# Kernel optimization log

Hardware: AMD Instinct MI355X
Metric: run time of the kernel (lower is better)

The kernel has to match this reference:

```python
import jax, jax.numpy as jnp
import numpy as np

D_HEAD = 128
H_Q = 16
H_K = 4
D_MODEL = 2048
B = 2
T = 2048


def setup_inputs() -> dict:
    key = jax.random.key(0)
    k1, k2, k3, k4, k5 = jax.random.split(key, 5)
    s = 0.02
    return {
        "x": jax.random.normal(k1, (B, T, D_MODEL), dtype=jnp.float32),
        "wq": jax.random.normal(k2, (D_HEAD * H_Q, D_MODEL), dtype=jnp.float32) * s,
        "wk": jax.random.normal(k3, (D_HEAD * H_K, D_MODEL), dtype=jnp.float32) * s,
        "wv": jax.random.normal(k4, (D_HEAD * H_K, D_MODEL), dtype=jnp.float32) * s,
        "wo": jax.random.normal(k5, (D_MODEL, D_HEAD * H_Q), dtype=jnp.float32) * s,
    }


def reference(x, wq, wk, wv, wo):
    Bs, Ts, _ = x.shape
    g = H_Q // H_K  # query groups per kv head
    # projections (torch Linear: y = x @ W^T)
    Q = (x @ wq.T).reshape(Bs, Ts, H_Q, D_HEAD).transpose(0, 2, 1, 3)  # [B,hq,T,d]
    K = (x @ wk.T).reshape(Bs, Ts, H_K, D_HEAD).transpose(0, 2, 1, 3)  # [B,hk,T,d]
    V = (x @ wv.T).reshape(Bs, Ts, H_K, D_HEAD).transpose(0, 2, 1, 3)  # [B,hk,T,d]
    Qg = Q.reshape(Bs, g, H_K, Ts, D_HEAD)  # [B,g,hk,T,d]
    scale = D_HEAD ** -0.5
    attn = jnp.einsum("bghtd,bhsd->bghts", Qg, K) * scale  # [B,g,hk,T,T]
    causal = jnp.tril(jnp.ones((Ts, Ts), dtype=bool))
    attn = jnp.where(causal, attn, -jnp.inf)
    attn = jax.nn.softmax(attn, axis=-1)
    out = jnp.einsum("bghts,bhsd->bghtd", attn, V)  # [B,g,hk,T,d]
    out = out.reshape(Bs, H_Q, Ts, D_HEAD).transpose(0, 2, 1, 3).reshape(Bs, Ts, H_Q * D_HEAD)
    return out @ wo.T
```

## Files before the change

kernel.cpp:

```cpp
#include <hip/hip_runtime.h>
#include <hip/hip_bf16.h>
#include <stdint.h>

#define DMODEL 2048
#define HQ 16
#define HKV 4
#define DH 128
#define SEQT 2048
#define BATCH 2

typedef __bf16 bf16x8 __attribute__((ext_vector_type(8)));
typedef float f32x4 __attribute__((ext_vector_type(4)));
typedef float f32x16 __attribute__((ext_vector_type(16)));
typedef unsigned short u16x4 __attribute__((ext_vector_type(4)));
typedef unsigned short u16x8 __attribute__((ext_vector_type(8)));

__device__ __forceinline__ unsigned short f2bf(float x) {
  __hip_bfloat16 h = __float2bfloat16(x);
  return __builtin_bit_cast(unsigned short, h);
}
__device__ __forceinline__ unsigned int pack2(float a, float b) {
  return (unsigned int)f2bf(a) | ((unsigned int)f2bf(b) << 16);
}

__device__ __forceinline__ void gload_lds16(const void* g, void* lds) {
  __builtin_amdgcn_global_load_lds(
      (const __attribute__((address_space(1))) void*)(uintptr_t)g,
      (__attribute__((address_space(3))) void*)(uint32_t)(uintptr_t)lds,
      16, 0, 0);
}

__global__ __launch_bounds__(256) void cast_all_kernel(
    const float* __restrict__ x, const float* __restrict__ wq,
    const float* __restrict__ wk, const float* __restrict__ wv,
    const float* __restrict__ wo,
    unsigned short* __restrict__ xb, unsigned short* __restrict__ wqb,
    unsigned short* __restrict__ wkb, unsigned short* __restrict__ wvb,
    unsigned short* __restrict__ wob) {
  int i = blockIdx.x * 256 + threadIdx.x;
  const float* in; unsigned short* out; int off; float s = 1.0f;
  if (i < 1048576)      { in = x;  out = xb;  off = i; }
  else if (i < 1572864) { in = wq; out = wqb; off = i - 1048576; s = 0.1275174473f; }
  else if (i < 1703936) { in = wk; out = wkb; off = i - 1572864; }
  else if (i < 1835008) { in = wv; out = wvb; off = i - 1703936; }
  else                  { in = wo; out = wob; off = i - 1835008; }
  const float4* p = reinterpret_cast<const float4*>(in) + (size_t)off * 2;
  float4 a = p[0], b = p[1];
  u16x8 o;
  o[0] = f2bf(a.x * s); o[1] = f2bf(a.y * s); o[2] = f2bf(a.z * s); o[3] = f2bf(a.w * s);
  o[4] = f2bf(b.x * s); o[5] = f2bf(b.y * s); o[6] = f2bf(b.z * s); o[7] = f2bf(b.w * s);
  *(reinterpret_cast<u16x8*>(out) + off) = o;
}

template <bool OUT_BF16>
__device__ __forceinline__ void gemm_body(
    unsigned short* As, unsigned short* Bs,
    const unsigned short* __restrict__ A, const unsigned short* __restrict__ B,
    void* __restrict__ Cv, int N, int K, int row0, int col0) {
  const int tid = threadIdx.x;
  const int wave = tid >> 6, lane = tid & 63;
  const int wr = (wave >> 1) * 64, wc = (wave & 1) * 64;
  const int l15 = lane & 15, l4 = lane >> 4;
  const int srow = wave * 32 + (lane >> 2);
  const int scol = (lane & 3) * 8;

  f32x4 acc[4][4] = {};

  for (int k0 = 0; k0 < K; k0 += 64) {
#pragma unroll
    for (int h = 0; h < 2; ++h) {
      const unsigned short* gA = A + (size_t)(row0 + srow) * K + k0 + h * 32 + scol;
      gload_lds16(gA, (char*)As + h * 8192 + wave * 2048);
      gload_lds16(gA + (size_t)16 * K, (char*)As + h * 8192 + wave * 2048 + 1024);
      const unsigned short* gB = B + (size_t)(col0 + srow) * K + k0 + h * 32 + scol;
      gload_lds16(gB, (char*)Bs + h * 8192 + wave * 2048);
      gload_lds16(gB + (size_t)16 * K, (char*)Bs + h * 8192 + wave * 2048 + 1024);
    }
    __syncthreads();

    bf16x8 af[2][4], bfr[2][4];
#pragma unroll
    for (int h = 0; h < 2; ++h)
#pragma unroll
      for (int i = 0; i < 4; ++i) {
        af[h][i]  = *reinterpret_cast<const bf16x8*>(&As[h * 4096 + (wr + i * 16 + l15) * 32 + l4 * 8]);
        bfr[h][i] = *reinterpret_cast<const bf16x8*>(&Bs[h * 4096 + (wc + i * 16 + l15) * 32 + l4 * 8]);
      }
#pragma unroll
    for (int h = 0; h < 2; ++h)
#pragma unroll
      for (int i = 0; i < 4; ++i)
#pragma unroll
        for (int j = 0; j < 4; ++j)
          acc[i][j] = __builtin_amdgcn_mfma_f32_16x16x32_bf16(af[h][i], bfr[h][j], acc[i][j], 0, 0, 0);
    __syncthreads();
  }

#pragma unroll
  for (int i = 0; i < 4; ++i) {
    const int rrow = row0 + wr + i * 16 + l4 * 4;
#pragma unroll
    for (int j = 0; j < 4; ++j) {
      const int ccol = col0 + wc + j * 16 + l15;
#pragma unroll
      for (int r = 0; r < 4; ++r) {
        const size_t idx = (size_t)(rrow + r) * N + ccol;
        if constexpr (OUT_BF16)
          ((unsigned short*)Cv)[idx] = f2bf(acc[i][j][r]);
        else
          ((float*)Cv)[idx] = acc[i][j][r];
      }
    }
  }
}

__global__ __launch_bounds__(256) void gemm_qkv(
    const unsigned short* __restrict__ xb, const unsigned short* __restrict__ wqb,
    const unsigned short* __restrict__ wkb, const unsigned short* __restrict__ wvb,
    unsigned short* __restrict__ Qb, unsigned short* __restrict__ Kb,
    unsigned short* __restrict__ VTb) {
  __shared__ alignas(16) unsigned short As[2][128 * 32];
  __shared__ alignas(16) unsigned short Bs[2][128 * 32];
  const int bid = blockIdx.x;
  if (bid < 512) {
    gemm_body<true>(&As[0][0], &Bs[0][0], xb, wqb, Qb, 2048, DMODEL,
                    (bid >> 4) * 128, (bid & 15) * 128);
  } else if (bid < 640) {
    const int r = bid - 512;
    gemm_body<true>(&As[0][0], &Bs[0][0], xb, wkb, Kb, 512, DMODEL,
                    (r >> 2) * 128, (r & 3) * 128);
  } else {
    const int r = bid - 640;
    const int tz = r & 1, ty = (r >> 1) & 15, tx = r >> 5;
    gemm_body<true>(&As[0][0], &Bs[0][0], wvb,
                    xb + (size_t)tz * SEQT * DMODEL,
                    VTb + (size_t)tz * 512 * SEQT, SEQT, DMODEL,
                    tx * 128, ty * 128);
  }
}

template <bool OUT_BF16>
__global__ __launch_bounds__(256) void gemm_bt(
    const unsigned short* __restrict__ A, const unsigned short* __restrict__ B,
    void* __restrict__ Cv, int N, int K) {
  __shared__ alignas(16) unsigned short As[2][128 * 32];
  __shared__ alignas(16) unsigned short Bs[2][128 * 32];
  gemm_body<OUT_BF16>(&As[0][0], &Bs[0][0], A, B, Cv, N, K,
                      blockIdx.x * 128, blockIdx.y * 128);
}

__device__ __forceinline__ void tile_pass(
    const char* ksb, const char* vsb, int lane, int hi, int lq,
    int kvb, int q0, const bf16x8* qf, f32x16* acc, float& mrun, float& lrun) {
  const bool s1v = (kvb + 32 <= q0);
  const bool d0 = (kvb == q0), d1 = (kvb + 32 == q0);

  f32x16 st0 = {}, st1 = {};
  __builtin_amdgcn_s_setprio(1);
#pragma unroll
  for (int dc = 0; dc < 8; ++dc) {
    bf16x8 kf = *reinterpret_cast<const bf16x8*>(ksb + dc * 1024 + lane * 16);
    st0 = __builtin_amdgcn_mfma_f32_32x32x16_bf16(kf, qf[dc], st0, 0, 0, 0);
  }
  if (s1v) {
#pragma unroll
    for (int dc = 0; dc < 8; ++dc) {
      bf16x8 kf = *reinterpret_cast<const bf16x8*>(ksb + (8 + dc) * 1024 + lane * 16);
      st1 = __builtin_amdgcn_mfma_f32_32x32x16_bf16(kf, qf[dc], st1, 0, 0, 0);
    }
  }
  __builtin_amdgcn_s_setprio(0);

  float p0[16], p1[16];
#pragma unroll
  for (int r = 0; r < 16; ++r) p0[r] = st0[r];
  if (d0) {
#pragma unroll
    for (int r = 0; r < 16; ++r) {
      const int srw = (r & 3) + 8 * (r >> 2) + 4 * hi;
      if (srw > lq) p0[r] = -INFINITY;
    }
  }
  float tmax = -INFINITY;
#pragma unroll
  for (int r = 0; r < 16; ++r) tmax = fmaxf(tmax, p0[r]);
  if (s1v) {
#pragma unroll
    for (int r = 0; r < 16; ++r) p1[r] = st1[r];
    if (d1) {
#pragma unroll
      for (int r = 0; r < 16; ++r) {
        const int srw = (r & 3) + 8 * (r >> 2) + 4 * hi;
        if (srw > lq) p1[r] = -INFINITY;
      }
    }
#pragma unroll
    for (int r = 0; r < 16; ++r) tmax = fmaxf(tmax, p1[r]);
  }
  tmax = fmaxf(tmax, __shfl_xor(tmax, 32));
  if (!__all(tmax <= mrun)) {
    const float mnew = fmaxf(mrun, tmax);
    const float fsc = __builtin_amdgcn_exp2f(mrun - mnew);
    lrun *= fsc;
#pragma unroll
    for (int dt = 0; dt < 4; ++dt)
#pragma unroll
      for (int r = 0; r < 16; ++r) acc[dt][r] *= fsc;
    mrun = mnew;
  }
  float psum = 0.f;
#pragma unroll
  for (int r = 0; r < 16; ++r) { p0[r] = __builtin_amdgcn_exp2f(p0[r] - mrun); psum += p0[r]; }
  if (s1v) {
#pragma unroll
    for (int r = 0; r < 16; ++r) { p1[r] = __builtin_amdgcn_exp2f(p1[r] - mrun); psum += p1[r]; }
  }
  psum += __shfl_xor(psum, 32);
  lrun += psum;

  union { unsigned int u[4]; bf16x8 v; } pf0, pf1, pf2, pf3;
  {
    unsigned int x0 = pack2(p0[0], p0[1]),  x1 = pack2(p0[2], p0[3]);
    unsigned int x2 = pack2(p0[4], p0[5]),  x3 = pack2(p0[6], p0[7]);
    unsigned int x4 = pack2(p0[8], p0[9]),  x5 = pack2(p0[10], p0[11]);
    unsigned int x6 = pack2(p0[12], p0[13]), x7 = pack2(p0[14], p0[15]);
    unsigned int x0s = __shfl_xor(x0, 32), x1s = __shfl_xor(x1, 32);
    unsigned int x2s = __shfl_xor(x2, 32), x3s = __shfl_xor(x3, 32);
    unsigned int x4s = __shfl_xor(x4, 32), x5s = __shfl_xor(x5, 32);
    unsigned int x6s = __shfl_xor(x6, 32), x7s = __shfl_xor(x7, 32);
    pf0.u[0] = hi ? x2s : x0;  pf0.u[1] = hi ? x3s : x1;
    pf0.u[2] = hi ? x2  : x0s; pf0.u[3] = hi ? x3  : x1s;
    pf1.u[0] = hi ? x6s : x4;  pf1.u[1] = hi ? x7s : x5;
    pf1.u[2] = hi ? x6  : x4s; pf1.u[3] = hi ? x7  : x5s;
  }
  if (s1v) {
    unsigned int x0 = pack2(p1[0], p1[1]),  x1 = pack2(p1[2], p1[3]);
    unsigned int x2 = pack2(p1[4], p1[5]),  x3 = pack2(p1[6], p1[7]);
    unsigned int x4 = pack2(p1[8], p1[9]),  x5 = pack2(p1[10], p1[11]);
    unsigned int x6 = pack2(p1[12], p1[13]), x7 = pack2(p1[14], p1[15]);
    unsigned int x0s = __shfl_xor(x0, 32), x1s = __shfl_xor(x1, 32);
    unsigned int x2s = __shfl_xor(x2, 32), x3s = __shfl_xor(x3, 32);
    unsigned int x4s = __shfl_xor(x4, 32), x5s = __shfl_xor(x5, 32);
    unsigned int x6s = __shfl_xor(x6, 32), x7s = __shfl_xor(x7, 32);
    pf2.u[0] = hi ? x2s : x0;  pf2.u[1] = hi ? x3s : x1;
    pf2.u[2] = hi ? x2  : x0s; pf2.u[3] = hi ? x3  : x1s;
    pf3.u[0] = hi ? x6s : x4;  pf3.u[1] = hi ? x7s : x5;
    pf3.u[2] = hi ? x6  : x4s; pf3.u[3] = hi ? x7  : x5s;
  }

  __builtin_amdgcn_s_setprio(1);
#pragma unroll
  for (int dt = 0; dt < 4; ++dt) {
    bf16x8 v0 = *reinterpret_cast<const bf16x8*>(vsb + (dt * 4 + 0) * 1024 + lane * 16);
    bf16x8 v1 = *reinterpret_cast<const bf16x8*>(vsb + (dt * 4 + 1) * 1024 + lane * 16);
    acc[dt] = __builtin_amdgcn_mfma_f32_32x32x16_bf16(v0, pf0.v, acc[dt], 0, 0, 0);
    acc[dt] = __builtin_amdgcn_mfma_f32_32x32x16_bf16(v1, pf1.v, acc[dt], 0, 0, 0);
  }
  if (s1v) {
#pragma unroll
    for (int dt = 0; dt < 4; ++dt) {
      bf16x8 v2 = *reinterpret_cast<const bf16x8*>(vsb + (dt * 4 + 2) * 1024 + lane * 16);
      bf16x8 v3 = *reinterpret_cast<const bf16x8*>(vsb + (dt * 4 + 3) * 1024 + lane * 16);
      acc[dt] = __builtin_amdgcn_mfma_f32_32x32x16_bf16(v2, pf2.v, acc[dt], 0, 0, 0);
      acc[dt] = __builtin_amdgcn_mfma_f32_32x32x16_bf16(v3, pf3.v, acc[dt], 0, 0, 0);
    }
  }
  __builtin_amdgcn_s_setprio(0);
}

__global__ __launch_bounds__(256, 1) void attn_kernel(
    const unsigned short* __restrict__ Q, const unsigned short* __restrict__ Kc,
    const unsigned short* __restrict__ VT, unsigned short* __restrict__ AO) {
  __shared__ alignas(16) unsigned short Ks[2][16 * 512];
  __shared__ alignas(16) unsigned short Vs[2][16 * 512];

  const int tid = threadIdx.x;
  const int wave = tid >> 6, lane = tid & 63;
  const int bid = blockIdx.x;
  const int bhk = bid & 7;
  const int pairidx = bid >> 3;
  const int b = bhk >> 2, hk = bhk & 3;
  const int h = hk + wave * 4;
  const int jl = 63 - pairidx, js = pairidx;
  const int q0l = jl * 32, q0s = js * 32;
  const int jtl = jl >> 1, jts = js >> 1;
  const int lq = lane & 31, hi = lane >> 5;

  const size_t qrowL = (size_t)(b * SEQT + q0l + lq);
  const size_t qrowS = (size_t)(b * SEQT + q0s + lq);
  bf16x8 qfL[8], qfS[8];
  {
    const unsigned short* qpL = Q + qrowL * (HQ * DH) + h * DH + hi * 8;
    const unsigned short* qpS = Q + qrowS * (HQ * DH) + h * DH + hi * 8;
#pragma unroll
    for (int dc = 0; dc < 8; ++dc) {
      qfL[dc] = *reinterpret_cast<const bf16x8*>(qpL + dc * 16);
      qfS[dc] = *reinterpret_cast<const bf16x8*>(qpS + dc * 16);
    }
  }

  f32x16 accL[4] = {}, accS[4] = {};
  float mL = -INFINITY, lL = 0.f, mS = -INFINITY, lS = 0.f;

  const unsigned short* kbase = Kc + (size_t)b * SEQT * (HKV * DH) + hk * DH;
  const unsigned short* vtb = VT + ((size_t)b * (HKV * DH) + hk * DH) * SEQT;

  auto STAGE = [&](int buf, int kvb2) {
#pragma unroll
    for (int i = 0; i < 4; ++i) {
      const int f = i * 4 + wave;
      const int sub = f >> 3, dc = f & 7;
      const unsigned short* g = kbase + (size_t)(kvb2 + sub * 32 + lq) * (HKV * DH) + dc * 16 + hi * 8;
      gload_lds16(g, (char*)Ks[buf] + f * 1024);
    }
#pragma unroll
    for (int i = 0; i < 4; ++i) {
      const int f = i * 4 + wave;
      const int dt = f >> 2, ks = f & 3;
      const unsigned short* g = vtb + (size_t)(dt * 32 + lq) * SEQT + kvb2 + ks * 16 + hi * 8;
      gload_lds16(g, (char*)Vs[buf] + f * 1024);
    }
  };

  STAGE(0, 0);
  __syncthreads();
  int cur = 0;

  for (int t = 0; t <= jtl; ++t) {
    if (t < jtl) STAGE(cur ^ 1, (t + 1) * 64);
    const char* ksb = (const char*)Ks[cur];
    const char* vsb = (const char*)Vs[cur];
    tile_pass(ksb, vsb, lane, hi, lq, t * 64, q0l, qfL, accL, mL, lL);
    if (t <= jts)
      tile_pass(ksb, vsb, lane, hi, lq, t * 64, q0s, qfS, accS, mS, lS);
    __syncthreads();
    cur ^= 1;
  }

  auto writeO = [&](const f32x16* acc, float lrun, size_t qrow) {
    const float inv = 1.f / lrun;
    unsigned short* op = AO + qrow * (HQ * DH) + h * DH;
#pragma unroll
    for (int dt = 0; dt < 4; ++dt) {
#pragma unroll
      for (int g2 = 0; g2 < 4; ++g2) {
        u16x4 w;
#pragma unroll
        for (int jj = 0; jj < 4; ++jj) w[jj] = f2bf(acc[dt][g2 * 4 + jj] * inv);
        *reinterpret_cast<u16x4*>(op + dt * 32 + g2 * 8 + 4 * hi) = w;
      }
    }
  };
  writeO(accL, lL, qrowL);
  writeO(accS, lS, qrowS);
}

extern "C" void kernel_launch(void* const* d_in, const int* in_sizes, int n_in,
                              void* d_out, int out_size, void* d_ws, size_t ws_size,
                              hipStream_t stream) {
  const float* x  = (const float*)d_in[0];
  const float* wq = (const float*)d_in[1];
  const float* wk = (const float*)d_in[2];
  const float* wv = (const float*)d_in[3];
  const float* wo = (const float*)d_in[4];
  float* out = (float*)d_out;

  const size_t N_X  = (size_t)BATCH * SEQT * DMODEL;
  const size_t N_WQ = (size_t)HQ * DH * DMODEL;
  const size_t N_WK = (size_t)HKV * DH * DMODEL;
  const size_t N_Q  = (size_t)BATCH * SEQT * HQ * DH;
  const size_t N_K  = (size_t)BATCH * SEQT * HKV * DH;

  unsigned short* xb  = (unsigned short*)d_ws;
  unsigned short* wqb = xb  + N_X;
  unsigned short* wkb = wqb + N_WQ;
  unsigned short* wvb = wkb + N_WK;
  unsigned short* wob = wvb + N_WK;
  unsigned short* Qb  = wob + N_WQ;
  unsigned short* Kb  = Qb  + N_Q;
  unsigned short* VTb = Kb  + N_K;
  unsigned short* AOb = VTb + N_K;

  cast_all_kernel<<<dim3(9216), dim3(256), 0, stream>>>(
      x, wq, wk, wv, wo, xb, wqb, wkb, wvb, wob);

  gemm_qkv<<<dim3(768), 256, 0, stream>>>(xb, wqb, wkb, wvb, Qb, Kb, VTb);
  attn_kernel<<<dim3(256, 1, 1), 256, 0, stream>>>(Qb, Kb, VTb, AOb);
  gemm_bt<false><<<dim3(32, 16, 1), 256, 0, stream>>>(AOb, wob, out, 2048, DMODEL);
}
```

Before: 211.1 us.

## Split paired-query attention blocks into single-tile blocks and load V from global

The attention kernel no longer has each block process a long and a short query tile together. It launches 512 blocks, each handling one 32-row query tile: long tiles are scheduled first and short tiles in a second round, with launch bounds raised to allow two blocks per CU. V fragments are now read directly from global memory into registers instead of being staged in LDS. The QK^T dot product is also split into two independent accumulator chains to expose more MFMA ILP. This trades the shared K/V reuse between paired tiles, plus some register headroom, for more occupancy and less LDS traffic.

New measurement: 269.6 us. 27.7% more time.

```diff
diff --git a/kernel.cpp b/kernel.cpp
--- a/kernel.cpp
+++ b/kernel.cpp
@@ -149,163 +149,38 @@
                       blockIdx.x * 128, blockIdx.y * 128);
 }
 
-__device__ __forceinline__ void tile_pass(
-    const char* ksb, const char* vsb, int lane, int hi, int lq,
-    int kvb, int q0, const bf16x8* qf, f32x16* acc, float& mrun, float& lrun) {
-  const bool s1v = (kvb + 32 <= q0);
-  const bool d0 = (kvb == q0), d1 = (kvb + 32 == q0);
-
-  f32x16 st0 = {}, st1 = {};
-  __builtin_amdgcn_s_setprio(1);
-#pragma unroll
-  for (int dc = 0; dc < 8; ++dc) {
-    bf16x8 kf = *reinterpret_cast<const bf16x8*>(ksb + dc * 1024 + lane * 16);
-    st0 = __builtin_amdgcn_mfma_f32_32x32x16_bf16(kf, qf[dc], st0, 0, 0, 0);
-  }
-  if (s1v) {
-#pragma unroll
-    for (int dc = 0; dc < 8; ++dc) {
-      bf16x8 kf = *reinterpret_cast<const bf16x8*>(ksb + (8 + dc) * 1024 + lane * 16);
-      st1 = __builtin_amdgcn_mfma_f32_32x32x16_bf16(kf, qf[dc], st1, 0, 0, 0);
-    }
-  }
-  __builtin_amdgcn_s_setprio(0);
-
-  float p0[16], p1[16];
-#pragma unroll
-  for (int r = 0; r < 16; ++r) p0[r] = st0[r];
-  if (d0) {
-#pragma unroll
-    for (int r = 0; r < 16; ++r) {
-      const int srw = (r & 3) + 8 * (r >> 2) + 4 * hi;
-      if (srw > lq) p0[r] = -INFINITY;
-    }
-  }
-  float tmax = -INFINITY;
-#pragma unroll
-  for (int r = 0; r < 16; ++r) tmax = fmaxf(tmax, p0[r]);
-  if (s1v) {
-#pragma unroll
-    for (int r = 0; r < 16; ++r) p1[r] = st1[r];
-    if (d1) {
-#pragma unroll
-      for (int r = 0; r < 16; ++r) {
-        const int srw = (r & 3) + 8 * (r >> 2) + 4 * hi;
-        if (srw > lq) p1[r] = -INFINITY;
-      }
-    }
-#pragma unroll
-    for (int r = 0; r < 16; ++r) tmax = fmaxf(tmax, p1[r]);
-  }
-  tmax = fmaxf(tmax, __shfl_xor(tmax, 32));
-  if (!__all(tmax <= mrun)) {
-    const float mnew = fmaxf(mrun, tmax);
-    const float fsc = __builtin_amdgcn_exp2f(mrun - mnew);
-    lrun *= fsc;
-#pragma unroll
-    for (int dt = 0; dt < 4; ++dt)
-#pragma unroll
-      for (int r = 0; r < 16; ++r) acc[dt][r] *= fsc;
-    mrun = mnew;
-  }
-  float psum = 0.f;
-#pragma unroll
-  for (int r = 0; r < 16; ++r) { p0[r] = __builtin_amdgcn_exp2f(p0[r] - mrun); psum += p0[r]; }
-  if (s1v) {
-#pragma unroll
-    for (int r = 0; r < 16; ++r) { p1[r] = __builtin_amdgcn_exp2f(p1[r] - mrun); psum += p1[r]; }
-  }
-  psum += __shfl_xor(psum, 32);
-  lrun += psum;
-
-  union { unsigned int u[4]; bf16x8 v; } pf0, pf1, pf2, pf3;
-  {
-    unsigned int x0 = pack2(p0[0], p0[1]),  x1 = pack2(p0[2], p0[3]);
-    unsigned int x2 = pack2(p0[4], p0[5]),  x3 = pack2(p0[6], p0[7]);
-    unsigned int x4 = pack2(p0[8], p0[9]),  x5 = pack2(p0[10], p0[11]);
-    unsigned int x6 = pack2(p0[12], p0[13]), x7 = pack2(p0[14], p0[15]);
-    unsigned int x0s = __shfl_xor(x0, 32), x1s = __shfl_xor(x1, 32);
-    unsigned int x2s = __shfl_xor(x2, 32), x3s = __shfl_xor(x3, 32);
-    unsigned int x4s = __shfl_xor(x4, 32), x5s = __shfl_xor(x5, 32);
-    unsigned int x6s = __shfl_xor(x6, 32), x7s = __shfl_xor(x7, 32);
-    pf0.u[0] = hi ? x2s : x0;  pf0.u[1] = hi ? x3s : x1;
-    pf0.u[2] = hi ? x2  : x0s; pf0.u[3] = hi ? x3  : x1s;
-    pf1.u[0] = hi ? x6s : x4;  pf1.u[1] = hi ? x7s : x5;
-    pf1.u[2] = hi ? x6  : x4s; pf1.u[3] = hi ? x7  : x5s;
-  }
-  if (s1v) {
-    unsigned int x0 = pack2(p1[0], p1[1]),  x1 = pack2(p1[2], p1[3]);
-    unsigned int x2 = pack2(p1[4], p1[5]),  x3 = pack2(p1[6], p1[7]);
-    unsigned int x4 = pack2(p1[8], p1[9]),  x5 = pack2(p1[10], p1[11]);
-    unsigned int x6 = pack2(p1[12], p1[13]), x7 = pack2(p1[14], p1[15]);
-    unsigned int x0s = __shfl_xor(x0, 32), x1s = __shfl_xor(x1, 32);
-    unsigned int x2s = __shfl_xor(x2, 32), x3s = __shfl_xor(x3, 32);
-    unsigned int x4s = __shfl_xor(x4, 32), x5s = __shfl_xor(x5, 32);
-    unsigned int x6s = __shfl_xor(x6, 32), x7s = __shfl_xor(x7, 32);
-    pf2.u[0] = hi ? x2s : x0;  pf2.u[1] = hi ? x3s : x1;
-    pf2.u[2] = hi ? x2  : x0s; pf2.u[3] = hi ? x3  : x1s;
-    pf3.u[0] = hi ? x6s : x4;  pf3.u[1] = hi ? x7s : x5;
-    pf3.u[2] = hi ? x6  : x4s; pf3.u[3] = hi ? x7  : x5s;
-  }
-
-  __builtin_amdgcn_s_setprio(1);
-#pragma unroll
-  for (int dt = 0; dt < 4; ++dt) {
-    bf16x8 v0 = *reinterpret_cast<const bf16x8*>(vsb + (dt * 4 + 0) * 1024 + lane * 16);
-    bf16x8 v1 = *reinterpret_cast<const bf16x8*>(vsb + (dt * 4 + 1) * 1024 + lane * 16);
-    acc[dt] = __builtin_amdgcn_mfma_f32_32x32x16_bf16(v0, pf0.v, acc[dt], 0, 0, 0);
-    acc[dt] = __builtin_amdgcn_mfma_f32_32x32x16_bf16(v1, pf1.v, acc[dt], 0, 0, 0);
-  }
-  if (s1v) {
-#pragma unroll
-    for (int dt = 0; dt < 4; ++dt) {
-      bf16x8 v2 = *reinterpret_cast<const bf16x8*>(vsb + (dt * 4 + 2) * 1024 + lane * 16);
-      bf16x8 v3 = *reinterpret_cast<const bf16x8*>(vsb + (dt * 4 + 3) * 1024 + lane * 16);
-      acc[dt] = __builtin_amdgcn_mfma_f32_32x32x16_bf16(v2, pf2.v, acc[dt], 0, 0, 0);
-      acc[dt] = __builtin_amdgcn_mfma_f32_32x32x16_bf16(v3, pf3.v, acc[dt], 0, 0, 0);
-    }
-  }
-  __builtin_amdgcn_s_setprio(0);
-}
-
-__global__ __launch_bounds__(256, 1) void attn_kernel(
+__global__ __launch_bounds__(256, 2) void attn_kernel(
     const unsigned short* __restrict__ Q, const unsigned short* __restrict__ Kc,
     const unsigned short* __restrict__ VT, unsigned short* __restrict__ AO) {
   __shared__ alignas(16) unsigned short Ks[2][16 * 512];
-  __shared__ alignas(16) unsigned short Vs[2][16 * 512];
 
   const int tid = threadIdx.x;
   const int wave = tid >> 6, lane = tid & 63;
   const int bid = blockIdx.x;
-  const int bhk = bid & 7;
-  const int pairidx = bid >> 3;
+  const int round = bid >> 8, pairslot = bid & 255;
+  const int bhk = pairslot & 7;
+  const int jp = pairslot >> 3;
+  const int j = round ? jp : 63 - jp;
   const int b = bhk >> 2, hk = bhk & 3;
   const int h = hk + wave * 4;
-  const int jl = 63 - pairidx, js = pairidx;
-  const int q0l = jl * 32, q0s = js * 32;
-  const int jtl = jl >> 1, jts = js >> 1;
+  const int q0 = j * 32;
+  const int jt = j >> 1;
   const int lq = lane & 31, hi = lane >> 5;
 
-  const size_t qrowL = (size_t)(b * SEQT + q0l + lq);
-  const size_t qrowS = (size_t)(b * SEQT + q0s + lq);
-  bf16x8 qfL[8], qfS[8];
-  {
-    const unsigned short* qpL = Q + qrowL * (HQ * DH) + h * DH + hi * 8;
-    const unsigned short* qpS = Q + qrowS * (HQ * DH) + h * DH + hi * 8;
-#pragma unroll
-    for (int dc = 0; dc < 8; ++dc) {
-      qfL[dc] = *reinterpret_cast<const bf16x8*>(qpL + dc * 16);
-      qfS[dc] = *reinterpret_cast<const bf16x8*>(qpS + dc * 16);
-    }
-  }
-
-  f32x16 accL[4] = {}, accS[4] = {};
-  float mL = -INFINITY, lL = 0.f, mS = -INFINITY, lS = 0.f;
+  const size_t qrow = (size_t)(b * SEQT + q0 + lq);
+  const unsigned short* qp = Q + qrow * (HQ * DH) + h * DH + hi * 8;
+  bf16x8 qf[8];
+#pragma unroll
+  for (int dc = 0; dc < 8; ++dc)
+    qf[dc] = *reinterpret_cast<const bf16x8*>(qp + dc * 16);
+
+  f32x16 acc[4] = {};
+  float mrun = -INFINITY, lrun = 0.f;
 
   const unsigned short* kbase = Kc + (size_t)b * SEQT * (HKV * DH) + hk * DH;
-  const unsigned short* vtb = VT + ((size_t)b * (HKV * DH) + hk * DH) * SEQT;
-
-  auto STAGE = [&](int buf, int kvb2) {
+  const unsigned short* vrow = VT + ((size_t)b * (HKV * DH) + hk * DH + lq) * SEQT + hi * 8;
+
+  auto STAGE_K = [&](int buf, int kvb2) {
 #pragma unroll
     for (int i = 0; i < 4; ++i) {
       const int f = i * 4 + wave;
@@ -313,46 +188,191 @@
       const unsigned short* g = kbase + (size_t)(kvb2 + sub * 32 + lq) * (HKV * DH) + dc * 16 + hi * 8;
       gload_lds16(g, (char*)Ks[buf] + f * 1024);
     }
-#pragma unroll
-    for (int i = 0; i < 4; ++i) {
-      const int f = i * 4 + wave;
-      const int dt = f >> 2, ks = f & 3;
-      const unsigned short* g = vtb + (size_t)(dt * 32 + lq) * SEQT + kvb2 + ks * 16 + hi * 8;
-      gload_lds16(g, (char*)Vs[buf] + f * 1024);
-    }
   };
 
-  STAGE(0, 0);
+  STAGE_K(0, 0);
   __syncthreads();
   int cur = 0;
 
-  for (int t = 0; t <= jtl; ++t) {
-    if (t < jtl) STAGE(cur ^ 1, (t + 1) * 64);
-    const char* ksb = (const char*)Ks[cur];
-    const char* vsb = (const char*)Vs[cur];
-    tile_pass(ksb, vsb, lane, hi, lq, t * 64, q0l, qfL, accL, mL, lL);
-    if (t <= jts)
-      tile_pass(ksb, vsb, lane, hi, lq, t * 64, q0s, qfS, accS, mS, lS);
+  for (int t = 0; t <= jt; ++t) {
+    const int kvb = t * 64;
+    const bool s1v = (kvb + 32 <= q0);
+    const bool d0 = (kvb == q0), d1 = (kvb + 32 == q0);
+
+    bf16x8 vfa[8];
+#pragma unroll
+    for (int dt = 0; dt < 4; ++dt)
+#pragma unroll
+      for (int ks = 0; ks < 2; ++ks)
+        vfa[dt * 2 + ks] = *reinterpret_cast<const bf16x8*>(
+            vrow + (size_t)dt * 32 * SEQT + kvb + ks * 16);
+
+    if (t < jt) STAGE_K(cur ^ 1, kvb + 64);
+
+    f32x16 stA = {}, stB = {}, stA1 = {}, stB1 = {};
+    __builtin_amdgcn_s_setprio(1);
+#pragma unroll
+    for (int dc = 0; dc < 4; ++dc) {
+      bf16x8 kf = *reinterpret_cast<const bf16x8*>((char*)Ks[cur] + dc * 1024 + lane * 16);
+      stA = __builtin_amdgcn_mfma_f32_32x32x16_bf16(kf, qf[dc], stA, 0, 0, 0);
+    }
+#pragma unroll
+    for (int dc = 4; dc < 8; ++dc) {
+      bf16x8 kf = *reinterpret_cast<const bf16x8*>((char*)Ks[cur] + dc * 1024 + lane * 16);
+      stB = __builtin_amdgcn_mfma_f32_32x32x16_bf16(kf, qf[dc], stB, 0, 0, 0);
+    }
+    if (s1v) {
+#pragma unroll
+      for (int dc = 0; dc < 4; ++dc) {
+        bf16x8 kf = *reinterpret_cast<const bf16x8*>((char*)Ks[cur] + (8 + dc) * 1024 + lane * 16);
+        stA1 = __builtin_amdgcn_mfma_f32_32x32x16_bf16(kf, qf[dc], stA1, 0, 0, 0);
+      }
+#pragma unroll
+      for (int dc = 4; dc < 8; ++dc) {
+        bf16x8 kf = *reinterpret_cast<const bf16x8*>((char*)Ks[cur] + (8 + dc) * 1024 + lane * 16);
+        stB1 = __builtin_amdgcn_mfma_f32_32x32x16_bf16(kf, qf[dc], stB1, 0, 0, 0);
+      }
+    }
+    __builtin_amdgcn_s_setprio(0);
+
+    bf16x8 vfb[8];
+    if (s1v) {
+#pragma unroll
+      for (int dt = 0; dt < 4; ++dt)
+#pragma unroll
+        for (int ks = 0; ks < 2; ++ks)
+          vfb[dt * 2 + ks] = *reinterpret_cast<const bf16x8*>(
+              vrow + (size_t)dt * 32 * SEQT + kvb + 32 + ks * 16);
+    }
+
+    float p0[16], p1[16];
+#pragma unroll
+    for (int r = 0; r < 16; ++r) p0[r] = stA[r] + stB[r];
+    if (d0) {
+#pragma unroll
+      for (int r = 0; r < 16; ++r) {
+        const int srw = (r & 3) + 8 * (r >> 2) + 4 * hi;
+        if (srw > lq) p0[r] = -INFINITY;
+      }
+    }
+    float m0, m1 = -INFINITY;
+    {
+      float a = fmaxf(fmaxf(p0[0], p0[1]), fmaxf(p0[2], p0[3]));
+      float bm = fmaxf(fmaxf(p0[4], p0[5]), fmaxf(p0[6], p0[7]));
+      float c = fmaxf(fmaxf(p0[8], p0[9]), fmaxf(p0[10], p0[11]));
+      float dm = fmaxf(fmaxf(p0[12], p0[13]), fmaxf(p0[14], p0[15]));
+      m0 = fmaxf(fmaxf(a, bm), fmaxf(c, dm));
+    }
+    if (s1v) {
+#pragma unroll
+      for (int r = 0; r < 16; ++r) p1[r] = stA1[r] + stB1[r];
+      if (d1) {
+#pragma unroll
+        for (int r = 0; r < 16; ++r) {
+          const int srw = (r & 3) + 8 * (r >> 2) + 4 * hi;
+          if (srw > lq) p1[r] = -INFINITY;
+        }
+      }
+      float a = fmaxf(fmaxf(p1[0], p1[1]), fmaxf(p1[2], p1[3]));
+      float bm = fmaxf(fmaxf(p1[4], p1[5]), fmaxf(p1[6], p1[7]));
+      float c = fmaxf(fmaxf(p1[8], p1[9]), fmaxf(p1[10], p1[11]));
+      float dm = fmaxf(fmaxf(p1[12], p1[13]), fmaxf(p1[14], p1[15]));
+      m1 = fmaxf(fmaxf(a, bm), fmaxf(c, dm));
+    }
+    float tmax = fmaxf(m0, m1);
+    tmax = fmaxf(tmax, __shfl_xor(tmax, 32));
+    if (!__all(tmax <= mrun)) {
+      const float mnew = fmaxf(mrun, tmax);
+      const float fsc = __builtin_amdgcn_exp2f(mrun - mnew);
+      lrun *= fsc;
+#pragma unroll
+      for (int dt = 0; dt < 4; ++dt)
+#pragma unroll
+        for (int r = 0; r < 16; ++r) acc[dt][r] *= fsc;
+      mrun = mnew;
+    }
+    float psum;
+    {
+#pragma unroll
+      for (int r = 0; r < 16; ++r) p0[r] = __builtin_amdgcn_exp2f(p0[r] - mrun);
+      float t0 = (p0[0] + p0[1]) + (p0[2] + p0[3]);
+      float t1 = (p0[4] + p0[5]) + (p0[6] + p0[7]);
+      float t2 = (p0[8] + p0[9]) + (p0[10] + p0[11]);
+      float t3 = (p0[12] + p0[13]) + (p0[14] + p0[15]);
+      psum = (t0 + t1) + (t2 + t3);
+    }
+    if (s1v) {
+#pragma unroll
+      for (int r = 0; r < 16; ++r) p1[r] = __builtin_amdgcn_exp2f(p1[r] - mrun);
+      float t0 = (p1[0] + p1[1]) + (p1[2] + p1[3]);
+      float t1 = (p1[4] + p1[5]) + (p1[6] + p1[7]);
+      float t2 = (p1[8] + p1[9]) + (p1[10] + p1[11]);
+      float t3 = (p1[12] + p1[13]) + (p1[14] + p1[15]);
+      psum += (t0 + t1) + (t2 + t3);
+    }
+    psum += __shfl_xor(psum, 32);
+    lrun += psum;
+
+    union { unsigned int u[4]; bf16x8 v; } pf0, pf1, pf2, pf3;
+    {
+      unsigned int x0 = pack2(p0[0], p0[1]),  x1 = pack2(p0[2], p0[3]);
+      unsigned int x2 = pack2(p0[4], p0[5]),  x3 = pack2(p0[6], p0[7]);
+      unsigned int x4 = pack2(p0[8], p0[9]),  x5 = pack2(p0[10], p0[11]);
+      unsigned int x6 = pack2(p0[12], p0[13]), x7 = pack2(p0[14], p0[15]);
+      unsigned int x0s = __shfl_xor(x0, 32), x1s = __shfl_xor(x1, 32);
+      unsigned int x2s = __shfl_xor(x2, 32), x3s = __shfl_xor(x3, 32);
+      unsigned int x4s = __shfl_xor(x4, 32), x5s = __shfl_xor(x5, 32);
+      unsigned int x6s = __shfl_xor(x6, 32), x7s = __shfl_xor(x7, 32);
+      pf0.u[0] = hi ? x2s : x0;  pf0.u[1] = hi ? x3s : x1;
+      pf0.u[2] = hi ? x2  : x0s; pf0.u[3] = hi ? x3  : x1s;
+      pf1.u[0] = hi ? x6s : x4;  pf1.u[1] = hi ? x7s : x5;
+      pf1.u[2] = hi ? x6  : x4s; pf1.u[3] = hi ? x7  : x5s;
+    }
+    if (s1v) {
+      unsigned int x0 = pack2(p1[0], p1[1]),  x1 = pack2(p1[2], p1[3]);
+      unsigned int x2 = pack2(p1[4], p1[5]),  x3 = pack2(p1[6], p1[7]);
+      unsigned int x4 = pack2(p1[8], p1[9]),  x5 = pack2(p1[10], p1[11]);
+      unsigned int x6 = pack2(p1[12], p1[13]), x7 = pack2(p1[14], p1[15]);
+      unsigned int x0s = __shfl_xor(x0, 32), x1s = __shfl_xor(x1, 32);
+      unsigned int x2s = __shfl_xor(x2, 32), x3s = __shfl_xor(x3, 32);
+      unsigned int x4s = __shfl_xor(x4, 32), x5s = __shfl_xor(x5, 32);
+      unsigned int x6s = __shfl_xor(x6, 32), x7s = __shfl_xor(x7, 32);
+      pf2.u[0] = hi ? x2s : x0;  pf2.u[1] = hi ? x3s : x1;
+      pf2.u[2] = hi ? x2  : x0s; pf2.u[3] = hi ? x3  : x1s;
+      pf3.u[0] = hi ? x6s : x4;  pf3.u[1] = hi ? x7s : x5;
+      pf3.u[2] = hi ? x6  : x4s; pf3.u[3] = hi ? x7  : x5s;
+    }
+
+    __builtin_amdgcn_s_setprio(1);
+#pragma unroll
+    for (int dt = 0; dt < 4; ++dt) {
+      acc[dt] = __builtin_amdgcn_mfma_f32_32x32x16_bf16(vfa[dt * 2 + 0], pf0.v, acc[dt], 0, 0, 0);
+      acc[dt] = __builtin_amdgcn_mfma_f32_32x32x16_bf16(vfa[dt * 2 + 1], pf1.v, acc[dt], 0, 0, 0);
+    }
+    if (s1v) {
+#pragma unroll
+      for (int dt = 0; dt < 4; ++dt) {
+        acc[dt] = __builtin_amdgcn_mfma_f32_32x32x16_bf16(vfb[dt * 2 + 0], pf2.v, acc[dt], 0, 0, 0);
+        acc[dt] = __builtin_amdgcn_mfma_f32_32x32x16_bf16(vfb[dt * 2 + 1], pf3.v, acc[dt], 0, 0, 0);
+      }
+    }
+    __builtin_amdgcn_s_setprio(0);
     __syncthreads();
     cur ^= 1;
   }
 
-  auto writeO = [&](const f32x16* acc, float lrun, size_t qrow) {
-    const float inv = 1.f / lrun;
-    unsigned short* op = AO + qrow * (HQ * DH) + h * DH;
-#pragma unroll
-    for (int dt = 0; dt < 4; ++dt) {
-#pragma unroll
-      for (int g2 = 0; g2 < 4; ++g2) {
-        u16x4 w;
-#pragma unroll
-        for (int jj = 0; jj < 4; ++jj) w[jj] = f2bf(acc[dt][g2 * 4 + jj] * inv);
-        *reinterpret_cast<u16x4*>(op + dt * 32 + g2 * 8 + 4 * hi) = w;
-      }
-    }
-  };
-  writeO(accL, lL, qrowL);
-  writeO(accS, lS, qrowS);
+  const float inv = 1.f / lrun;
+  unsigned short* op = AO + qrow * (HQ * DH) + h * DH;
+#pragma unroll
+  for (int dt = 0; dt < 4; ++dt) {
+#pragma unroll
+    for (int g2 = 0; g2 < 4; ++g2) {
+      u16x4 w;
+#pragma unroll
+      for (int jj = 0; jj < 4; ++jj) w[jj] = f2bf(acc[dt][g2 * 4 + jj] * inv);
+      *reinterpret_cast<u16x4*>(op + dt * 32 + g2 * 8 + 4 * hi) = w;
+    }
+  }
 }
 
 extern "C" void kernel_launch(void* const* d_in, const int* in_sizes, int n_in,
@@ -385,6 +405,6 @@
       x, wq, wk, wv, wo, xb, wqb, wkb, wvb, wob);
 
   gemm_qkv<<<dim3(768), 256, 0, stream>>>(xb, wqb, wkb, wvb, Qb, Kb, VTb);
-  attn_kernel<<<dim3(256, 1, 1), 256, 0, stream>>>(Qb, Kb, VTb, AOb);
+  attn_kernel<<<dim3(512, 1, 1), 256, 0, stream>>>(Qb, Kb, VTb, AOb);
   gemm_bt<false><<<dim3(32, 16, 1), 256, 0, stream>>>(AOb, wob, out, 2048, DMODEL);
 }
```
